# Performance work log

Measured on AMD Instinct MI355X. Metric: run time of the kernel, lower is better.

Reference implementation:

```python
import jax, jax.numpy as jnp
import numpy as np

B = 4096
D = 64  # emb_dim, hardcoded in UserEmb/ItemEmb


def setup_inputs() -> dict:
    key = jax.random.key(0)
    ks = jax.random.split(key, 26)
    n = lambda k, shape, s=1.0: jax.random.normal(k, shape, dtype=jnp.float32) * s
    inp = {
        'user_emb': jax.random.randint(ks[0], (B, 4), 0, 6, dtype=jnp.int32),
        'item_emb': jax.random.randint(ks[1], (B, 10242), 0, 2, dtype=jnp.int32),
        'edge_emb': jnp.zeros((B,), dtype=jnp.int32),  # edges_emb has num_embeddings=1
        # UserEmb params
        'gender_tab': n(ks[2], (98, D)),
        'age_tab': n(ks[3], (7, D)),
        'occ_tab': n(ks[4], (21, D)),
        'area_tab': n(ks[5], (3402, D)),
        'user_W': n(ks[6], (4 * D, D), 0.05),  # stored [in,out]
        'user_b': n(ks[7], (D,), 0.05),
        # ItemEmb params
        'rate_tab': n(ks[8], (6, D)),
        'genre_W': n(ks[9], (25, D), 0.05),
        'director_W': n(ks[10], (2186, D), 0.02),
        'actor_W': n(ks[11], (8030, D), 0.01),
        'item_W': n(ks[12], (4 * D, D), 0.05),
        'item_b': n(ks[13], (D,), 0.05),
        # GLNFeat params (torch: randn * 0.5)
        'edges_tab': n(ks[14], (1, D)),
        'uu_w': n(ks[15], (D,), 0.5),
        'ui_w': n(ks[16], (D,), 0.5),
        'iu_w': n(ks[17], (D,), 0.5),
        'ii_w': n(ks[18], (D,), 0.5),
        'edge_W': n(ks[19], (D, D), 0.5),
        'uu_W1': n(ks[20], (D, D), 0.5),
        'ui_W1': n(ks[21], (D, D), 0.5),
        'iu_W1': n(ks[22], (D, D), 0.5),
        'ii_W1': n(ks[23], (D, D), 0.5),
    }
    return inp


def _lrelu(v):
    return jnp.where(v >= 0, v, 0.01 * v)  # nn.LeakyReLU default slope


def reference(user_emb, item_emb, edge_emb, gender_tab, age_tab, occ_tab, area_tab,
              user_W, user_b, rate_tab, genre_W, director_W, actor_W, item_W, item_b,
              edges_tab, uu_w, ui_w, iu_w, ii_w, edge_W, uu_W1, ui_W1, iu_W1, ii_W1):
    a = 0.12
    b = 0.12
    # UserEmb
    u_cat = jnp.concatenate([gender_tab[user_emb[:, 0]], age_tab[user_emb[:, 1]],
                             occ_tab[user_emb[:, 2]], area_tab[user_emb[:, 3]]], axis=1)
    x = (u_cat @ user_W + user_b) * a  # [B, D]
    # ItemEmb: multi-hot fields projected then mean-normalized by count
    genre = item_emb[:, 1:26].astype(jnp.float32)
    director = item_emb[:, 26:2212].astype(jnp.float32)
    actor = item_emb[:, 2212:10242].astype(jnp.float32)
    ge = (genre @ genre_W) / jnp.sum(genre, 1, keepdims=True)
    de = (director @ director_W) / jnp.sum(director, 1, keepdims=True)
    ae = (actor @ actor_W) / jnp.sum(actor, 1, keepdims=True)
    i_cat = jnp.concatenate([rate_tab[item_emb[:, 0]], ge, de, ae], axis=1)
    y = (i_cat @ item_W + item_b) * a  # [B, D]
    edge = edges_tab[edge_emb] * b  # [B, D]

    def outer_mm(u, v, M):
        # stop_gradient(outer(u, v) @ M) == u[:,None] * (v @ M), avoids [B,B]
        return jax.lax.stop_gradient(u[:, None] * (v @ M))

    xe = x * edge
    ye = y * edge
    x_xx = xe @ uu_w      # [B]
    x_xy_x = xe @ ui_w
    x_xy_y = ye @ ui_w
    t1 = outer_mm(x_xx, x_xx, x)
    t2 = outer_mm(x_xy_x, x_xy_y, y)
    x_buy = (_lrelu(t1 @ uu_W1) + _lrelu(t2 @ ui_W1)) / 2
    y_yy = ye @ ii_w
    y_yx_y = ye @ iu_w
    y_yx_x = xe @ iu_w
    t3 = outer_mm(y_yy, y_yy, y)
    t4 = outer_mm(y_yx_y, y_yx_x, x)
    y_buy = (_lrelu(t3 @ ii_W1) + _lrelu(t4 @ iu_W1)) / 2
    new = _lrelu(edge @ edge_W)
    return ((x_buy + x) / 2, (y_buy + y) / 2, (new + edge) / 2)
```

## Files before the change

kernel.cpp:

```cpp
#include <hip/hip_runtime.h>
#include <cstddef>

constexpr int BATCH = 4096;
constexpr int ITEM_COLS = 10242;
constexpr int FBTK = 10304;

constexpr int R_GENDER = 0;
constexpr int R_AGE    = 98;
constexpr int R_OCC    = 105;
constexpr int R_AREA   = 126;
constexpr int R_RATE   = 3528;
constexpr int R_FU     = 3534;

constexpr size_t OFF_FU  = 0;
constexpr size_t OFF_NEW = OFF_FU + (size_t)R_FU * 64;
constexpr size_t OFF_FBT = OFF_NEW + 64;
constexpr size_t OFF_X   = OFF_FBT + (size_t)64 * FBTK / 2;
constexpr size_t OFF_Y   = OFF_X + (size_t)BATCH * 64;
constexpr size_t OFF_P   = OFF_Y + (size_t)BATCH * 64;
constexpr size_t OFF_C   = OFF_P + 9ull * BATCH * 64;
constexpr size_t OFF_SP  = OFF_C + 9ull * BATCH;
constexpr size_t OFF_PB  = OFF_SP + 256ull * 256;
constexpr size_t OFF_SC  = OFF_PB + 4ull * 64;

__device__ const int ASTART[9] = {1, 25, 1113, 2209, 3545, 4881, 6225, 7561, 8897};
__device__ const int VSTART[9] = {1, 26, 1119, 2212, 3550, 4888, 6227, 7565, 8903};
__device__ const int VEND[9]   = {26, 1119, 2212, 3550, 4888, 6227, 7565, 8903, 10242};

typedef __attribute__((ext_vector_type(8))) short bf16x8;
typedef __attribute__((ext_vector_type(4))) float f32x4;

__device__ __forceinline__ float lrelu(float v) { return v >= 0.0f ? v : 0.01f * v; }

__device__ __forceinline__ short bf_trunc(float f) {
    return (short)(__builtin_bit_cast(unsigned, f) >> 16);
}
__device__ __forceinline__ unsigned bf_rne_pair(float lo, float hi) {
    unsigned ul = __builtin_bit_cast(unsigned, lo);
    unsigned uh = __builtin_bit_cast(unsigned, hi);
    ul += 0x7fffu + ((ul >> 16) & 1u);
    uh += 0x7fffu + ((uh >> 16) & 1u);
    return (ul >> 16) | (uh & 0xffff0000u);
}

__global__ __launch_bounds__(256) void k_fuseA(
        const float* __restrict__ gender_tab, const float* __restrict__ age_tab,
        const float* __restrict__ occ_tab, const float* __restrict__ area_tab,
        const float* __restrict__ user_W, const float* __restrict__ rate_tab,
        const float* __restrict__ item_W, const float* __restrict__ edges_tab,
        const float* __restrict__ edge_W, float* __restrict__ Fu, float* __restrict__ NEWt) {
    int t = threadIdx.x;
    int n = t & 63;
    int rb = __builtin_amdgcn_readfirstlane(t >> 6);
    int r = blockIdx.x * 4 + rb;
    if (r > R_FU) return;
    if (r == R_FU) {
        float acc = 0.0f;
#pragma unroll
        for (int k = 0; k < 64; ++k)
            acc = fmaf(edges_tab[k] * 0.12f, edge_W[k * 64 + n], acc);
        NEWt[n] = lrelu(acc);
        return;
    }
    const float* src;
    const float* W;
    if (r < R_AGE)       { src = gender_tab + (size_t)r * 64;            W = user_W;            }
    else if (r < R_OCC)  { src = age_tab    + (size_t)(r - R_AGE) * 64;  W = user_W + 64 * 64;  }
    else if (r < R_AREA) { src = occ_tab    + (size_t)(r - R_OCC) * 64;  W = user_W + 128 * 64; }
    else if (r < R_RATE) { src = area_tab   + (size_t)(r - R_AREA) * 64; W = user_W + 192 * 64; }
    else                 { src = rate_tab   + (size_t)(r - R_RATE) * 64; W = item_W;            }
    float acc = 0.0f;
#pragma unroll
    for (int k = 0; k < 64; ++k)
        acc = fmaf(src[k], W[k * 64 + n], acc);
    Fu[(size_t)r * 64 + n] = acc;
}

__global__ __launch_bounds__(256) void k_fuseT(
        const float* __restrict__ genre_W, const float* __restrict__ director_W,
        const float* __restrict__ actor_W, const float* __restrict__ item_W,
        short* __restrict__ Fbt) {
    const int t = threadIdx.x;
    const int KT0 = blockIdx.x * 64;
    const int n = t & 63;
    const int rb = __builtin_amdgcn_readfirstlane(t >> 6);
    __shared__ float T[64 * 65];
    for (int rl = 0; rl < 16; ++rl) {
        int r = rl * 4 + rb;
        int KT = KT0 + r;
        float acc = 0.0f;
        if (KT < 10241) {
            const float* src;
            const float* W;
            if (KT < 25)        { src = genre_W    + (size_t)KT * 64;          W = item_W + 64 * 64;  }
            else if (KT < 2211) { src = director_W + (size_t)(KT - 25) * 64;   W = item_W + 128 * 64; }
            else                { src = actor_W    + (size_t)(KT - 2211) * 64; W = item_W + 192 * 64; }
#pragma unroll
            for (int k = 0; k < 64; ++k)
                acc = fmaf(src[k], W[k * 64 + n], acc);
        }
        T[r * 65 + n] = acc;
    }
    __syncthreads();
    int n2 = t >> 2, sg = t & 3;
    unsigned dw[8];
#pragma unroll
    for (int d = 0; d < 8; ++d)
        dw[d] = bf_rne_pair(T[(sg * 16 + 2 * d) * 65 + n2], T[(sg * 16 + 2 * d + 1) * 65 + n2]);
    uint4* dst = (uint4*)(Fbt + (size_t)n2 * FBTK + KT0 + sg * 16);
    dst[0] = make_uint4(dw[0], dw[1], dw[2], dw[3]);
    dst[1] = make_uint4(dw[4], dw[5], dw[6], dw[7]);
}

__global__ __launch_bounds__(256) void k_item(const int* __restrict__ item,
                                              const short* __restrict__ Fbt,
                                              float* __restrict__ P, float* __restrict__ C) {
    const int ch = blockIdx.y;
    const int astart = ASTART[ch], vs = VSTART[ch], ve = VEND[ch];
    const int len = ve - astart;
    const int KT0 = astart - 1;
    const int m0 = blockIdx.x * 64;
    const int t = threadIdx.x;
    const int lane = t & 63;
    const int w = __builtin_amdgcn_readfirstlane(t >> 6);
    const int q = lane >> 4, r16 = lane & 15;

    __shared__ short As[64 * 136];
    __shared__ short Bs[64 * 136];

    f32x4 acc[5];
#pragma unroll
    for (int s = 0; s < 5; ++s) acc[s] = (f32x4){0.f, 0.f, 0.f, 0.f};

    short o = (r16 == 0) ? (short)0x3f80 : (short)0;
    bf16x8 ones = {o, o, o, o, o, o, o, o};

    for (int kb = 0; kb < len; kb += 128) {
        __syncthreads();
        const int c0 = astart + kb;
        if (c0 >= vs && c0 + 128 <= ve) {
#pragma unroll
            for (int it = 0; it < 32; ++it) {
                int f = it * 256 + t;
                int r = f >> 7, cc = f & 127;
                int v = item[(size_t)(m0 + r) * ITEM_COLS + c0 + cc];
                As[r * 136 + cc] = bf_trunc((float)v);
            }
        } else {
#pragma unroll
            for (int it = 0; it < 32; ++it) {
                int f = it * 256 + t;
                int r = f >> 7, cc = f & 127;
                int c = c0 + cc;
                int v = (c >= vs && c < ve) ? item[(size_t)(m0 + r) * ITEM_COLS + c] : 0;
                As[r * 136 + cc] = bf_trunc((float)v);
            }
        }
        {
            int nB = t >> 2, pt = t & 3;
            const short* fb = Fbt + (size_t)nB * FBTK + KT0 + kb;
#pragma unroll
            for (int p = 0; p < 4; ++p) {
                int off = (p * 4 + pt) * 8;
                *(uint4*)(Bs + nB * 136 + off) = *(const uint4*)(fb + off);
            }
        }
        __syncthreads();
#pragma unroll
        for (int kt = 0; kt < 4; ++kt) {
            bf16x8 a = *(const bf16x8*)(As + (w * 16 + r16) * 136 + kt * 32 + q * 8);
#pragma unroll
            for (int s = 0; s < 4; ++s) {
                bf16x8 b = *(const bf16x8*)(Bs + (s * 16 + r16) * 136 + kt * 32 + q * 8);
                acc[s] = __builtin_amdgcn_mfma_f32_16x16x32_bf16(a, b, acc[s], 0, 0, 0);
            }
            acc[4] = __builtin_amdgcn_mfma_f32_16x16x32_bf16(a, ones, acc[4], 0, 0, 0);
        }
    }
    const size_t pb = (size_t)ch * BATCH + m0 + w * 16 + q * 4;
#pragma unroll
    for (int reg = 0; reg < 4; ++reg) {
        float* pr = P + (pb + reg) * 64 + r16;
        pr[0] = acc[0][reg];
        pr[16] = acc[1][reg];
        pr[32] = acc[2][reg];
        pr[48] = acc[3][reg];
    }
    if (r16 == 0) {
#pragma unroll
        for (int reg = 0; reg < 4; ++reg)
            C[(size_t)ch * BATCH + m0 + w * 16 + q * 4 + reg] = acc[4][reg];
    }
}

__device__ __forceinline__ float wred(float v) {
#pragma unroll
    for (int m = 1; m < 64; m <<= 1) v += __shfl_xor(v, m, 64);
    return v;
}

__global__ __launch_bounds__(256) void k_mid(const int* __restrict__ item, const int* __restrict__ edge_emb,
                                             const int* __restrict__ user_emb,
                                             const float* __restrict__ Fu, const float* __restrict__ user_b,
                                             const float* __restrict__ P, const float* __restrict__ C,
                                             const float* __restrict__ item_b, const float* __restrict__ edges_tab,
                                             const float* __restrict__ uu_w, const float* __restrict__ ui_w,
                                             const float* __restrict__ iu_w, const float* __restrict__ ii_w,
                                             float* __restrict__ X, float* __restrict__ Y,
                                             float* __restrict__ SC, float* __restrict__ SP) {
    const int t = threadIdx.x;
    const int n = t & 63;
    const int wv = __builtin_amdgcn_readfirstlane(t >> 6);
    const float uuw = uu_w[n], uiw = ui_w[n], iuw = iu_w[n], iiw = ii_w[n];
    const float ib = item_b[n], ub = user_b[n];
    const size_t cs = (size_t)BATCH * 64;
    float s1 = 0.0f, s2 = 0.0f, s3 = 0.0f, s4 = 0.0f;

    for (int i = 0; i < 4; ++i) {
        int b = blockIdx.x * 16 + wv * 4 + i;
        const int* ue = user_emb + (size_t)b * 4;
        float x = (Fu[(size_t)(R_GENDER + ue[0]) * 64 + n]
                 + Fu[(size_t)(R_AGE    + ue[1]) * 64 + n]
                 + Fu[(size_t)(R_OCC    + ue[2]) * 64 + n]
                 + Fu[(size_t)(R_AREA   + ue[3]) * 64 + n] + ub) * 0.12f;
        X[(size_t)b * 64 + n] = x;
        int ri = item[(size_t)b * ITEM_COLS];
        size_t base = (size_t)b * 64 + n;
        float sg = P[base];
        float sd = P[base + cs] + P[base + 2 * cs];
        float sa = P[base + 3 * cs] + P[base + 4 * cs] + P[base + 5 * cs]
                 + P[base + 6 * cs] + P[base + 7 * cs] + P[base + 8 * cs];
        float cg = C[b];
        float cd = C[BATCH + b] + C[2 * BATCH + b];
        float ca = C[3 * BATCH + b] + C[4 * BATCH + b] + C[5 * BATCH + b]
                 + C[6 * BATCH + b] + C[7 * BATCH + b] + C[8 * BATCH + b];
        float y = (Fu[(size_t)(R_RATE + ri) * 64 + n] + sg / cg + sd / cd + sa / ca + ib) * 0.12f;
        Y[(size_t)b * 64 + n] = y;
        float e = edges_tab[(size_t)edge_emb[b] * 64 + n] * 0.12f;
        float xe = x * e, ye = y * e;
        float r1 = wred(xe * uuw);
        float r2 = wred(xe * uiw);
        float r3 = wred(xe * iuw);
        float r4 = wred(ye * uiw);
        float r5 = wred(ye * iiw);
        float r6 = wred(ye * iuw);
        if (n == 0) {
            SC[b] = r1; SC[BATCH + b] = r2; SC[2 * BATCH + b] = r5; SC[3 * BATCH + b] = r6;
        }
        s1 = fmaf(r1, x, s1);
        s2 = fmaf(r4, y, s2);
        s3 = fmaf(r5, y, s3);
        s4 = fmaf(r3, x, s4);
    }
    __shared__ float sp[4][4][64];
    sp[wv][0][n] = s1; sp[wv][1][n] = s2; sp[wv][2][n] = s3; sp[wv][3][n] = s4;
    __syncthreads();
    int i2 = t >> 6;
    float v = sp[0][i2][n] + sp[1][i2][n] + sp[2][i2][n] + sp[3][i2][n];
    SP[(size_t)blockIdx.x * 256 + t] = v;
}

__global__ __launch_bounds__(1024) void k_red(const float* __restrict__ SP,
                                              const float* __restrict__ uu_W1, const float* __restrict__ ui_W1,
                                              const float* __restrict__ iu_W1, const float* __restrict__ ii_W1,
                                              float* __restrict__ PB) {
    int t = threadIdx.x;
    int sub = t >> 8, i = (t >> 6) & 3, n = t & 63;
    float s = 0.0f;
    for (int wb = sub * 64; wb < sub * 64 + 64; ++wb)
        s += SP[(size_t)wb * 256 + i * 64 + n];
    __shared__ float red[4][4][64];
    red[sub][i][n] = s;
    __syncthreads();
    float sv = red[0][i][n] + red[1][i][n] + red[2][i][n] + red[3][i][n];
    __shared__ float sl[4][64];
    if (t < 256) sl[i][n] = sv;
    __syncthreads();
    if (t < 256) {
        const float* W1 = (i == 0) ? uu_W1 : (i == 1) ? ui_W1 : (i == 2) ? ii_W1 : iu_W1;
        float p = 0.0f;
#pragma unroll
        for (int k = 0; k < 64; ++k) p = fmaf(sl[i][k], W1[k * 64 + n], p);
        PB[i * 64 + n] = p;
    }
}

__global__ __launch_bounds__(256) void k_out(const float* __restrict__ X, const float* __restrict__ Y,
                                             const float* __restrict__ SC, const float* __restrict__ PB,
                                             const float* __restrict__ NEWt, const float* __restrict__ edges_tab,
                                             const int* __restrict__ edge_emb, float* __restrict__ out) {
    int t = threadIdx.x;
    int b = blockIdx.x * 4 + (t >> 6);
    int n = t & 63;
    float xx = SC[b], xyx = SC[BATCH + b], yy = SC[2 * BATCH + b], yxy = SC[3 * BATCH + b];
    float p1 = PB[n], p2 = PB[64 + n], p3 = PB[128 + n], p4 = PB[192 + n];
    float x = X[(size_t)b * 64 + n], y = Y[(size_t)b * 64 + n];
    float o1 = ((lrelu(xx * p1) + lrelu(xyx * p2)) * 0.5f + x) * 0.5f;
    float o2 = ((lrelu(yy * p3) + lrelu(yxy * p4)) * 0.5f + y) * 0.5f;
    int ei = edge_emb[b];
    float e = edges_tab[(size_t)ei * 64 + n] * 0.12f;
    float o3 = (NEWt[n] + e) * 0.5f;
    out[(size_t)b * 64 + n] = o1;
    out[((size_t)BATCH + b) * 64 + n] = o2;
    out[((size_t)2 * BATCH + b) * 64 + n] = o3;
}

extern "C" void kernel_launch(void* const* d_in, const int* in_sizes, int n_in,
                              void* d_out, int out_size, void* d_ws, size_t ws_size,
                              hipStream_t stream) {
    (void)in_sizes; (void)n_in; (void)out_size; (void)ws_size;
    const int*   user_emb   = (const int*)  d_in[0];
    const int*   item_emb   = (const int*)  d_in[1];
    const int*   edge_emb   = (const int*)  d_in[2];
    const float* gender_tab = (const float*)d_in[3];
    const float* age_tab    = (const float*)d_in[4];
    const float* occ_tab    = (const float*)d_in[5];
    const float* area_tab   = (const float*)d_in[6];
    const float* user_W     = (const float*)d_in[7];
    const float* user_b     = (const float*)d_in[8];
    const float* rate_tab   = (const float*)d_in[9];
    const float* genre_W    = (const float*)d_in[10];
    const float* director_W = (const float*)d_in[11];
    const float* actor_W    = (const float*)d_in[12];
    const float* item_W     = (const float*)d_in[13];
    const float* item_b     = (const float*)d_in[14];
    const float* edges_tab  = (const float*)d_in[15];
    const float* uu_w       = (const float*)d_in[16];
    const float* ui_w       = (const float*)d_in[17];
    const float* iu_w       = (const float*)d_in[18];
    const float* ii_w       = (const float*)d_in[19];
    const float* edge_W     = (const float*)d_in[20];
    const float* uu_W1      = (const float*)d_in[21];
    const float* ui_W1      = (const float*)d_in[22];
    const float* iu_W1      = (const float*)d_in[23];
    const float* ii_W1      = (const float*)d_in[24];

    float* ws   = (float*)d_ws;
    float* Fu   = ws + OFF_FU;
    float* NEWt = ws + OFF_NEW;
    short* Fbt  = (short*)(ws + OFF_FBT);
    float* X    = ws + OFF_X;
    float* Y    = ws + OFF_Y;
    float* P    = ws + OFF_P;
    float* C    = ws + OFF_C;
    float* SP   = ws + OFF_SP;
    float* PB   = ws + OFF_PB;
    float* SC   = ws + OFF_SC;
    float* out  = (float*)d_out;

    hipLaunchKernelGGL(k_fuseA, dim3(884), dim3(256), 0, stream,
                       gender_tab, age_tab, occ_tab, area_tab, user_W, rate_tab,
                       item_W, edges_tab, edge_W, Fu, NEWt);
    hipLaunchKernelGGL(k_fuseT, dim3(FBTK / 64), dim3(256), 0, stream,
                       genre_W, director_W, actor_W, item_W, Fbt);
    hipLaunchKernelGGL(k_item, dim3(BATCH / 64, 9), dim3(256), 0, stream, item_emb, Fbt, P, C);
    hipLaunchKernelGGL(k_mid, dim3(BATCH / 16), dim3(256), 0, stream,
                       item_emb, edge_emb, user_emb, Fu, user_b, P, C, item_b, edges_tab,
                       uu_w, ui_w, iu_w, ii_w, X, Y, SC, SP);
    hipLaunchKernelGGL(k_red, dim3(1), dim3(1024), 0, stream, SP, uu_W1, ui_W1, iu_W1, ii_W1, PB);
    hipLaunchKernelGGL(k_out, dim3(BATCH / 4), dim3(256), 0, stream,
                       X, Y, SC, PB, NEWt, edges_tab, edge_emb, out);
}
```

Baseline: 355.0 us.

## Merge fuse kernels, repartition item GEMM into aligned chunks, read B from global

Combines the two precompute kernels into a single launch with a block-index branch. Repartitions the multi-hot item GEMM into 15 K-chunks aligned to 128-column tiles, raising grid parallelism and reducing padded work. Drops the shared-memory staging of the B operand in favour of direct global/L2 loads into MFMA operands, and swaps the float-to-bf16 conversion for a simple 0/1 select. Direct global B loads may raise memory latency per MFMA, and the mid kernel now sums more partials.

```diff
diff --git a/kernel.cpp b/kernel.cpp
--- a/kernel.cpp
+++ b/kernel.cpp
@@ -4,6 +4,7 @@
 constexpr int BATCH = 4096;
 constexpr int ITEM_COLS = 10242;
 constexpr int FBTK = 10304;
+constexpr int NPART = 15;
 
 constexpr int R_GENDER = 0;
 constexpr int R_AGE    = 98;
@@ -18,23 +19,21 @@
 constexpr size_t OFF_X   = OFF_FBT + (size_t)64 * FBTK / 2;
 constexpr size_t OFF_Y   = OFF_X + (size_t)BATCH * 64;
 constexpr size_t OFF_P   = OFF_Y + (size_t)BATCH * 64;
-constexpr size_t OFF_C   = OFF_P + 9ull * BATCH * 64;
-constexpr size_t OFF_SP  = OFF_C + 9ull * BATCH;
+constexpr size_t OFF_C   = OFF_P + (size_t)NPART * BATCH * 64;
+constexpr size_t OFF_SP  = OFF_C + (size_t)NPART * BATCH;
 constexpr size_t OFF_PB  = OFF_SP + 256ull * 256;
 constexpr size_t OFF_SC  = OFF_PB + 4ull * 64;
 
-__device__ const int ASTART[9] = {1, 25, 1113, 2209, 3545, 4881, 6225, 7561, 8897};
-__device__ const int VSTART[9] = {1, 26, 1119, 2212, 3550, 4888, 6227, 7565, 8903};
-__device__ const int VEND[9]   = {26, 1119, 2212, 3550, 4888, 6227, 7565, 8903, 10242};
+__device__ const int AST[NPART] = {0, 24, 792, 1560, 2208, 2976, 3744, 4512, 5280, 6048, 6816, 7584, 8352, 9120, 9888};
+__device__ const int VS [NPART] = {0, 25, 792, 1560, 2211, 2976, 3744, 4512, 5280, 6048, 6816, 7584, 8352, 9120, 9888};
+__device__ const int VE [NPART] = {25, 792, 1560, 2211, 2976, 3744, 4512, 5280, 6048, 6816, 7584, 8352, 9120, 9888, 10241};
+__device__ const int PLEN[NPART] = {128, 768, 768, 768, 768, 768, 768, 768, 768, 768, 768, 768, 768, 768, 384};
 
 typedef __attribute__((ext_vector_type(8))) short bf16x8;
 typedef __attribute__((ext_vector_type(4))) float f32x4;
 
 __device__ __forceinline__ float lrelu(float v) { return v >= 0.0f ? v : 0.01f * v; }
 
-__device__ __forceinline__ short bf_trunc(float f) {
-    return (short)(__builtin_bit_cast(unsigned, f) >> 16);
-}
 __device__ __forceinline__ unsigned bf_rne_pair(float lo, float hi) {
     unsigned ul = __builtin_bit_cast(unsigned, lo);
     unsigned uh = __builtin_bit_cast(unsigned, hi);
@@ -43,45 +42,44 @@
     return (ul >> 16) | (uh & 0xffff0000u);
 }
 
-__global__ __launch_bounds__(256) void k_fuseA(
+__global__ __launch_bounds__(256) void k_fuse(
         const float* __restrict__ gender_tab, const float* __restrict__ age_tab,
         const float* __restrict__ occ_tab, const float* __restrict__ area_tab,
         const float* __restrict__ user_W, const float* __restrict__ rate_tab,
-        const float* __restrict__ item_W, const float* __restrict__ edges_tab,
-        const float* __restrict__ edge_W, float* __restrict__ Fu, float* __restrict__ NEWt) {
-    int t = threadIdx.x;
-    int n = t & 63;
-    int rb = __builtin_amdgcn_readfirstlane(t >> 6);
-    int r = blockIdx.x * 4 + rb;
-    if (r > R_FU) return;
-    if (r == R_FU) {
-        float acc = 0.0f;
-#pragma unroll
-        for (int k = 0; k < 64; ++k)
-            acc = fmaf(edges_tab[k] * 0.12f, edge_W[k * 64 + n], acc);
-        NEWt[n] = lrelu(acc);
-        return;
-    }
-    const float* src;
-    const float* W;
-    if (r < R_AGE)       { src = gender_tab + (size_t)r * 64;            W = user_W;            }
-    else if (r < R_OCC)  { src = age_tab    + (size_t)(r - R_AGE) * 64;  W = user_W + 64 * 64;  }
-    else if (r < R_AREA) { src = occ_tab    + (size_t)(r - R_OCC) * 64;  W = user_W + 128 * 64; }
-    else if (r < R_RATE) { src = area_tab   + (size_t)(r - R_AREA) * 64; W = user_W + 192 * 64; }
-    else                 { src = rate_tab   + (size_t)(r - R_RATE) * 64; W = item_W;            }
-    float acc = 0.0f;
-#pragma unroll
-    for (int k = 0; k < 64; ++k)
-        acc = fmaf(src[k], W[k * 64 + n], acc);
-    Fu[(size_t)r * 64 + n] = acc;
-}
-
-__global__ __launch_bounds__(256) void k_fuseT(
         const float* __restrict__ genre_W, const float* __restrict__ director_W,
         const float* __restrict__ actor_W, const float* __restrict__ item_W,
-        short* __restrict__ Fbt) {
+        const float* __restrict__ edges_tab, const float* __restrict__ edge_W,
+        float* __restrict__ Fu, float* __restrict__ NEWt, short* __restrict__ Fbt) {
     const int t = threadIdx.x;
-    const int KT0 = blockIdx.x * 64;
+    const int bx = blockIdx.x;
+    if (bx < 884) {
+        int n = t & 63;
+        int rb = __builtin_amdgcn_readfirstlane(t >> 6);
+        int r = bx * 4 + rb;
+        if (r > R_FU) return;
+        if (r == R_FU) {
+            float acc = 0.0f;
+#pragma unroll
+            for (int k = 0; k < 64; ++k)
+                acc = fmaf(edges_tab[k] * 0.12f, edge_W[k * 64 + n], acc);
+            NEWt[n] = lrelu(acc);
+            return;
+        }
+        const float* src;
+        const float* W;
+        if (r < R_AGE)       { src = gender_tab + (size_t)r * 64;            W = user_W;            }
+        else if (r < R_OCC)  { src = age_tab    + (size_t)(r - R_AGE) * 64;  W = user_W + 64 * 64;  }
+        else if (r < R_AREA) { src = occ_tab    + (size_t)(r - R_OCC) * 64;  W = user_W + 128 * 64; }
+        else if (r < R_RATE) { src = area_tab   + (size_t)(r - R_AREA) * 64; W = user_W + 192 * 64; }
+        else                 { src = rate_tab   + (size_t)(r - R_RATE) * 64; W = item_W;            }
+        float acc = 0.0f;
+#pragma unroll
+        for (int k = 0; k < 64; ++k)
+            acc = fmaf(src[k], W[k * 64 + n], acc);
+        Fu[(size_t)r * 64 + n] = acc;
+        return;
+    }
+    const int KT0 = (bx - 884) * 64;
     const int n = t & 63;
     const int rb = __builtin_amdgcn_readfirstlane(t >> 6);
     __shared__ float T[64 * 65];
@@ -115,10 +113,8 @@
 __global__ __launch_bounds__(256) void k_item(const int* __restrict__ item,
                                               const short* __restrict__ Fbt,
                                               float* __restrict__ P, float* __restrict__ C) {
-    const int ch = blockIdx.y;
-    const int astart = ASTART[ch], vs = VSTART[ch], ve = VEND[ch];
-    const int len = ve - astart;
-    const int KT0 = astart - 1;
+    const int part = blockIdx.y;
+    const int ast = AST[part], vs = VS[part], ve = VE[part], len = PLEN[part];
     const int m0 = blockIdx.x * 64;
     const int t = threadIdx.x;
     const int lane = t & 63;
@@ -126,58 +122,49 @@
     const int q = lane >> 4, r16 = lane & 15;
 
     __shared__ short As[64 * 136];
-    __shared__ short Bs[64 * 136];
 
     f32x4 acc[5];
 #pragma unroll
     for (int s = 0; s < 5; ++s) acc[s] = (f32x4){0.f, 0.f, 0.f, 0.f};
 
-    short o = (r16 == 0) ? (short)0x3f80 : (short)0;
-    bf16x8 ones = {o, o, o, o, o, o, o, o};
+    const short o = (r16 == 0) ? (short)0x3f80 : (short)0;
+    const bf16x8 ones = {o, o, o, o, o, o, o, o};
 
     for (int kb = 0; kb < len; kb += 128) {
         __syncthreads();
-        const int c0 = astart + kb;
-        if (c0 >= vs && c0 + 128 <= ve) {
+        const int K0 = ast + kb;
+        if (K0 >= vs && K0 + 128 <= ve) {
 #pragma unroll
             for (int it = 0; it < 32; ++it) {
                 int f = it * 256 + t;
                 int r = f >> 7, cc = f & 127;
-                int v = item[(size_t)(m0 + r) * ITEM_COLS + c0 + cc];
-                As[r * 136 + cc] = bf_trunc((float)v);
+                int v = item[(size_t)(m0 + r) * ITEM_COLS + 1 + K0 + cc];
+                As[r * 136 + cc] = v ? (short)0x3f80 : (short)0;
             }
         } else {
 #pragma unroll
             for (int it = 0; it < 32; ++it) {
                 int f = it * 256 + t;
                 int r = f >> 7, cc = f & 127;
-                int c = c0 + cc;
-                int v = (c >= vs && c < ve) ? item[(size_t)(m0 + r) * ITEM_COLS + c] : 0;
-                As[r * 136 + cc] = bf_trunc((float)v);
+                int KT = K0 + cc;
+                int v = (KT >= vs && KT < ve) ? item[(size_t)(m0 + r) * ITEM_COLS + 1 + KT] : 0;
+                As[r * 136 + cc] = v ? (short)0x3f80 : (short)0;
             }
         }
-        {
-            int nB = t >> 2, pt = t & 3;
-            const short* fb = Fbt + (size_t)nB * FBTK + KT0 + kb;
-#pragma unroll
-            for (int p = 0; p < 4; ++p) {
-                int off = (p * 4 + pt) * 8;
-                *(uint4*)(Bs + nB * 136 + off) = *(const uint4*)(fb + off);
-            }
-        }
         __syncthreads();
+        const short* fb = Fbt + K0 + (size_t)q * 8;
 #pragma unroll
         for (int kt = 0; kt < 4; ++kt) {
             bf16x8 a = *(const bf16x8*)(As + (w * 16 + r16) * 136 + kt * 32 + q * 8);
 #pragma unroll
             for (int s = 0; s < 4; ++s) {
-                bf16x8 b = *(const bf16x8*)(Bs + (s * 16 + r16) * 136 + kt * 32 + q * 8);
+                bf16x8 b = *(const bf16x8*)(fb + (size_t)(s * 16 + r16) * FBTK + kt * 32);
                 acc[s] = __builtin_amdgcn_mfma_f32_16x16x32_bf16(a, b, acc[s], 0, 0, 0);
             }
             acc[4] = __builtin_amdgcn_mfma_f32_16x16x32_bf16(a, ones, acc[4], 0, 0, 0);
         }
     }
-    const size_t pb = (size_t)ch * BATCH + m0 + w * 16 + q * 4;
+    const size_t pb = (size_t)part * BATCH + m0 + w * 16 + q * 4;
 #pragma unroll
     for (int reg = 0; reg < 4; ++reg) {
         float* pr = P + (pb + reg) * 64 + r16;
@@ -189,7 +176,7 @@
     if (r16 == 0) {
 #pragma unroll
         for (int reg = 0; reg < 4; ++reg)
-            C[(size_t)ch * BATCH + m0 + w * 16 + q * 4 + reg] = acc[4][reg];
+            C[(size_t)part * BATCH + m0 + w * 16 + q * 4 + reg] = acc[4][reg];
     }
 }
 
@@ -226,14 +213,12 @@
         X[(size_t)b * 64 + n] = x;
         int ri = item[(size_t)b * ITEM_COLS];
         size_t base = (size_t)b * 64 + n;
-        float sg = P[base];
-        float sd = P[base + cs] + P[base + 2 * cs];
-        float sa = P[base + 3 * cs] + P[base + 4 * cs] + P[base + 5 * cs]
-                 + P[base + 6 * cs] + P[base + 7 * cs] + P[base + 8 * cs];
-        float cg = C[b];
-        float cd = C[BATCH + b] + C[2 * BATCH + b];
-        float ca = C[3 * BATCH + b] + C[4 * BATCH + b] + C[5 * BATCH + b]
-                 + C[6 * BATCH + b] + C[7 * BATCH + b] + C[8 * BATCH + b];
+        float sg = P[base], cg = C[b];
+        float sd = 0.0f, cd = 0.0f, sa = 0.0f, ca = 0.0f;
+#pragma unroll
+        for (int p2 = 1; p2 < 4; ++p2)  { sd += P[base + p2 * cs]; cd += C[p2 * BATCH + b]; }
+#pragma unroll
+        for (int p2 = 4; p2 < 15; ++p2) { sa += P[base + p2 * cs]; ca += C[p2 * BATCH + b]; }
         float y = (Fu[(size_t)(R_RATE + ri) * 64 + n] + sg / cg + sd / cd + sa / ca + ib) * 0.12f;
         Y[(size_t)b * 64 + n] = y;
         float e = edges_tab[(size_t)edge_emb[b] * 64 + n] * 0.12f;
@@ -297,8 +282,7 @@
     float x = X[(size_t)b * 64 + n], y = Y[(size_t)b * 64 + n];
     float o1 = ((lrelu(xx * p1) + lrelu(xyx * p2)) * 0.5f + x) * 0.5f;
     float o2 = ((lrelu(yy * p3) + lrelu(yxy * p4)) * 0.5f + y) * 0.5f;
-    int ei = edge_emb[b];
-    float e = edges_tab[(size_t)ei * 64 + n] * 0.12f;
+    float e = edges_tab[(size_t)edge_emb[b] * 64 + n] * 0.12f;
     float o3 = (NEWt[n] + e) * 0.5f;
     out[(size_t)b * 64 + n] = o1;
     out[((size_t)BATCH + b) * 64 + n] = o2;
@@ -348,12 +332,10 @@
     float* SC   = ws + OFF_SC;
     float* out  = (float*)d_out;
 
-    hipLaunchKernelGGL(k_fuseA, dim3(884), dim3(256), 0, stream,
+    hipLaunchKernelGGL(k_fuse, dim3(884 + FBTK / 64), dim3(256), 0, stream,
                        gender_tab, age_tab, occ_tab, area_tab, user_W, rate_tab,
-                       item_W, edges_tab, edge_W, Fu, NEWt);
-    hipLaunchKernelGGL(k_fuseT, dim3(FBTK / 64), dim3(256), 0, stream,
-                       genre_W, director_W, actor_W, item_W, Fbt);
-    hipLaunchKernelGGL(k_item, dim3(BATCH / 64, 9), dim3(256), 0, stream, item_emb, Fbt, P, C);
+                       genre_W, director_W, actor_W, item_W, edges_tab, edge_W, Fu, NEWt, Fbt);
+    hipLaunchKernelGGL(k_item, dim3(BATCH / 64, NPART), dim3(256), 0, stream, item_emb, Fbt, P, C);
     hipLaunchKernelGGL(k_mid, dim3(BATCH / 16), dim3(256), 0, stream,
                        item_emb, edge_emb, user_emb, Fu, user_b, P, C, item_b, edges_tab,
                        uu_w, ui_w, iu_w, ii_w, X, Y, SC, SP);
```

Measured after the change: 357.7 us. Within noise of the previous version (+0.8%).
